# Kernel optimization log

Measured on AMD Instinct MI355X. Metric: run time of the kernel, lower is better.

Reference implementation:

```python
import jax, jax.numpy as jnp
import numpy as np

EPS = 1e-08


def squash(x):
    # x: [..., D]; scale by ||x||^2/(1+||x||^2) and normalize by ||x||
    lengths2 = jnp.sum(x * x, axis=-1, keepdims=True)
    lengths = jnp.sqrt(lengths2)
    return x * (lengths2 / (1.0 + lengths2)) / (lengths + EPS)


def setup_inputs() -> dict:
    key = jax.random.key(0)
    k1, = jax.random.split(key, 1)
    B, G, S, O, D = 32, 8, 1152, 10, 16
    u_predict = jax.random.normal(k1, (B, G, S, O, D), dtype=jnp.float32)
    b_param = jnp.zeros((G, 1, S, O), dtype=jnp.float32)
    return {"u_predict": u_predict, "b_param": b_param, "n_iterations": 3}


def reference(u_predict, b_param, n_iterations):
    B, G, S, O, D = u_predict.shape
    # b: expand param (G,1,S,O) -> (G,B,S,O), permute -> (B,G,S,O)
    b = jnp.transpose(jnp.broadcast_to(b_param, (G, B, S, O)), (1, 0, 2, 3))
    v = None
    for r in range(n_iterations):
        c = jax.nn.softmax(b, axis=3)[..., None]          # [B,G,S,O,1]
        s = jnp.sum(c * u_predict, axis=2)                # [B,G,O,D]
        v = squash(s)                                     # [B,G,O,D]
        if r < n_iterations - 1:
            # agreement: dot(u_predict, v) over D
            b = b + jnp.sum(u_predict * v[:, :, None], axis=-1)  # [B,G,S,O]
    return jnp.sum(v, axis=1)                             # [B,O,D]
```

## Files before the change

kernel.cpp:

```cpp
#include <hip/hip_runtime.h>

#define NB 32
#define NG 8
#define NS 1152
#define NO 10
#define ND 16
#define EPSV 1e-8f

#define THREADS 512
#define NWAVES (THREADS / 64)
#define GRPS (THREADS / 4)
#define NSTEPS (NS / GRPS)

__global__ __launch_bounds__(THREADS)
void AgreementRouting_72988674228343_kernel(const float* __restrict__ u,
                                            const float* __restrict__ b_param,
                                            const int* __restrict__ n_iter_p,
                                            float* __restrict__ out) {
    __shared__ float  b_lds[NS * NO];
    __shared__ float4 sred[NWAVES][NO][4];
    __shared__ float4 v_lds[NO][4];

    const int tid  = threadIdx.x;
    const int blk  = blockIdx.x;
    const int g    = blk & (NG - 1);
    const int bb   = blk >> 3;
    const int wave = tid >> 6;
    const int lane = tid & 63;
    const int d4   = tid & 3;
    const int grp  = tid >> 2;

    const int n_iter = n_iter_p[0];

    const float* bp = b_param + (size_t)g * (NS * NO);
    for (int i = tid; i < NS * NO; i += THREADS) b_lds[i] = bp[i];

    const float4* ub = (const float4*)u + (size_t)blk * (NS * NO * ND / 4);

    float4 v[NO];
    __syncthreads();

    for (int r = 0; r < n_iter; ++r) {
        float4 sacc[NO];
#pragma unroll
        for (int o = 0; o < NO; ++o) sacc[o] = make_float4(0.f, 0.f, 0.f, 0.f);

        for (int step = 0; step < NSTEPS; ++step) {
            const int s = step * GRPS + grp;
            const float4* row = ub + (size_t)s * (NO * 4) + d4;
            float4 uu[NO];
#pragma unroll
            for (int o = 0; o < NO; ++o) uu[o] = row[o * 4];

            float bnew[NO];
            if (r > 0) {
                float p[NO];
#pragma unroll
                for (int o = 0; o < NO; ++o)
                    p[o] = uu[o].x * v[o].x + uu[o].y * v[o].y +
                           uu[o].z * v[o].z + uu[o].w * v[o].w;
#pragma unroll
                for (int o = 0; o < NO; ++o) {
                    p[o] += __shfl_xor(p[o], 1);
                    p[o] += __shfl_xor(p[o], 2);
                    bnew[o] = b_lds[s * NO + o] + p[o];
                }
#pragma unroll
                for (int o = 0; o < NO; ++o)
                    if ((o & 3) == d4) b_lds[s * NO + o] = bnew[o];
            } else {
#pragma unroll
                for (int o = 0; o < NO; ++o) bnew[o] = b_lds[s * NO + o];
            }

            float m = bnew[0];
#pragma unroll
            for (int o = 1; o < NO; ++o) m = fmaxf(m, bnew[o]);
            float e[NO]; float ssum = 0.f;
#pragma unroll
            for (int o = 0; o < NO; ++o) { e[o] = __expf(bnew[o] - m); ssum += e[o]; }
            const float inv = 1.f / ssum;
#pragma unroll
            for (int o = 0; o < NO; ++o) {
                const float c = e[o] * inv;
                sacc[o].x += c * uu[o].x;
                sacc[o].y += c * uu[o].y;
                sacc[o].z += c * uu[o].z;
                sacc[o].w += c * uu[o].w;
            }
        }

#pragma unroll
        for (int o = 0; o < NO; ++o) {
#pragma unroll
            for (int mask = 4; mask <= 32; mask <<= 1) {
                sacc[o].x += __shfl_xor(sacc[o].x, mask);
                sacc[o].y += __shfl_xor(sacc[o].y, mask);
                sacc[o].z += __shfl_xor(sacc[o].z, mask);
                sacc[o].w += __shfl_xor(sacc[o].w, mask);
            }
        }
        if (lane < 4) {
#pragma unroll
            for (int o = 0; o < NO; ++o) sred[wave][o][lane] = sacc[o];
        }
        __syncthreads();

        if (tid < NO * 4) {
            const int o = tid >> 2, dd = tid & 3;
            float4 sv = sred[0][o][dd];
#pragma unroll
            for (int w = 1; w < NWAVES; ++w) {
                float4 t = sred[w][o][dd];
                sv.x += t.x; sv.y += t.y; sv.z += t.z; sv.w += t.w;
            }
            float q = sv.x * sv.x + sv.y * sv.y + sv.z * sv.z + sv.w * sv.w;
            q += __shfl_xor(q, 1);
            q += __shfl_xor(q, 2);
            const float len = sqrtf(q);
            const float f = (q / (1.f + q)) / (len + EPSV);
            const float4 vv = make_float4(sv.x * f, sv.y * f, sv.z * f, sv.w * f);
            v_lds[o][dd] = vv;
            if (r == n_iter - 1) {
                float* op = out + (size_t)bb * (NO * ND) + o * ND + dd * 4;
                atomicAdd(op + 0, vv.x);
                atomicAdd(op + 1, vv.y);
                atomicAdd(op + 2, vv.z);
                atomicAdd(op + 3, vv.w);
            }
        }
        __syncthreads();
#pragma unroll
        for (int o = 0; o < NO; ++o) v[o] = v_lds[o][d4];
    }
}

extern "C" void kernel_launch(void* const* d_in, const int* in_sizes, int n_in,
                              void* d_out, int out_size, void* d_ws, size_t ws_size,
                              hipStream_t stream) {
    const float* u   = (const float*)d_in[0];
    const float* bp  = (const float*)d_in[1];
    const int*   nit = (const int*)d_in[2];
    float* out = (float*)d_out;

    hipMemsetAsync(out, 0, (size_t)out_size * sizeof(float), stream);

    AgreementRouting_72988674228343_kernel<<<dim3(NB * NG), dim3(THREADS), 0, stream>>>(
        u, bp, nit, out);
}
```

Baseline: 318.7 us.

## Stage an fp16 copy of u_predict for later routing iterations

```diff
diff --git a/kernel.cpp b/kernel.cpp
--- a/kernel.cpp
+++ b/kernel.cpp
@@ -1,4 +1,6 @@
 #include <hip/hip_runtime.h>
+#include <hip/hip_fp16.h>
+#include <stdint.h>
 
 #define NB 32
 #define NG 8
@@ -8,81 +10,107 @@
 #define EPSV 1e-8f
 
 #define THREADS 512
-#define NWAVES (THREADS / 64)
 #define GRPS (THREADS / 4)
 #define NSTEPS (NS / GRPS)
+#define UHROW (NO * 4)
+
+typedef float f4v __attribute__((ext_vector_type(4)));
 
 __global__ __launch_bounds__(THREADS)
 void AgreementRouting_72988674228343_kernel(const float* __restrict__ u,
-                                            const float* __restrict__ b_param,
+                                            const float* __restrict__ bparam,
                                             const int* __restrict__ n_iter_p,
-                                            float* __restrict__ out) {
+                                            float* __restrict__ out,
+                                            uint2* __restrict__ uh)
+{
     __shared__ float  b_lds[NS * NO];
-    __shared__ float4 sred[NWAVES][NO][4];
+    __shared__ float4 sred[8][NO][4];
     __shared__ float4 v_lds[NO][4];
 
     const int tid  = threadIdx.x;
-    const int blk  = blockIdx.x;
-    const int g    = blk & (NG - 1);
-    const int bb   = blk >> 3;
+    const int bg   = blockIdx.x;
+    const int g    = bg & 7;
+    const int bb   = bg >> 3;
     const int wave = tid >> 6;
     const int lane = tid & 63;
     const int d4   = tid & 3;
     const int grp  = tid >> 2;
 
-    const int n_iter = n_iter_p[0];
+    const int n = n_iter_p[0];
 
-    const float* bp = b_param + (size_t)g * (NS * NO);
+    const float* bp = bparam + (size_t)g * (NS * NO);
     for (int i = tid; i < NS * NO; i += THREADS) b_lds[i] = bp[i];
+    if (tid < NO * 4) v_lds[tid >> 2][tid & 3] = make_float4(0.f, 0.f, 0.f, 0.f);
 
-    const float4* ub = (const float4*)u + (size_t)blk * (NS * NO * ND / 4);
+    const f4v* ub  = (const f4v*)u + (size_t)bg * (NS * NO * 4);
+    uint2*     uhb = uh + (size_t)bg * (NS * UHROW);
 
-    float4 v[NO];
     __syncthreads();
 
-    for (int r = 0; r < n_iter; ++r) {
+    for (int r = 0; r < n; ++r) {
         float4 sacc[NO];
 #pragma unroll
         for (int o = 0; o < NO; ++o) sacc[o] = make_float4(0.f, 0.f, 0.f, 0.f);
 
         for (int step = 0; step < NSTEPS; ++step) {
             const int s = step * GRPS + grp;
-            const float4* row = ub + (size_t)s * (NO * 4) + d4;
             float4 uu[NO];
+            float bnew[NO];
+
+            if (r == 0) {
+                const f4v* row = ub + (size_t)s * (NO * 4) + d4;
+                f4v t[NO];
 #pragma unroll
-            for (int o = 0; o < NO; ++o) uu[o] = row[o * 4];
-
-            float bnew[NO];
-            if (r > 0) {
-                float p[NO];
+                for (int o = 0; o < NO; ++o) t[o] = __builtin_nontemporal_load(row + o * 4);
+                if (n > 1) {
+                    uint2* wrow = uhb + (size_t)s * UHROW + d4;
 #pragma unroll
-                for (int o = 0; o < NO; ++o)
-                    p[o] = uu[o].x * v[o].x + uu[o].y * v[o].y +
-                           uu[o].z * v[o].z + uu[o].w * v[o].w;
+                    for (int o = 0; o < NO; ++o) {
+                        const __half2 lo = __floats2half2_rn(t[o].x, t[o].y);
+                        const __half2 hi = __floats2half2_rn(t[o].z, t[o].w);
+                        uint2 pk;
+                        pk.x = __builtin_bit_cast(uint32_t, lo);
+                        pk.y = __builtin_bit_cast(uint32_t, hi);
+                        wrow[o * 4] = pk;
+                    }
+                }
 #pragma unroll
                 for (int o = 0; o < NO; ++o) {
-                    p[o] += __shfl_xor(p[o], 1);
-                    p[o] += __shfl_xor(p[o], 2);
-                    bnew[o] = b_lds[s * NO + o] + p[o];
+                    uu[o] = make_float4(t[o].x, t[o].y, t[o].z, t[o].w);
+                    bnew[o] = b_lds[s * NO + o];
+                }
+            } else {
+                const uint2* row = uhb + (size_t)s * UHROW + d4;
+                uint2 pk[NO];
+#pragma unroll
+                for (int o = 0; o < NO; ++o) pk[o] = row[o * 4];
+#pragma unroll
+                for (int o = 0; o < NO; ++o) {
+                    const float2 a = __half22float2(__builtin_bit_cast(__half2, pk[o].x));
+                    const float2 b = __half22float2(__builtin_bit_cast(__half2, pk[o].y));
+                    uu[o] = make_float4(a.x, a.y, b.x, b.y);
                 }
 #pragma unroll
-                for (int o = 0; o < NO; ++o)
-                    if ((o & 3) == d4) b_lds[s * NO + o] = bnew[o];
-            } else {
-#pragma unroll
-                for (int o = 0; o < NO; ++o) bnew[o] = b_lds[s * NO + o];
+                for (int o = 0; o < NO; ++o) {
+                    const float4 vc = v_lds[o][d4];
+                    float p = uu[o].x * vc.x + uu[o].y * vc.y +
+                              uu[o].z * vc.z + uu[o].w * vc.w;
+                    p += __shfl_xor(p, 1);
+                    p += __shfl_xor(p, 2);
+                    bnew[o] = b_lds[s * NO + o] + p;
+                }
             }
 
-            float m = bnew[0];
+            float mx = bnew[0];
 #pragma unroll
-            for (int o = 1; o < NO; ++o) m = fmaxf(m, bnew[o]);
-            float e[NO]; float ssum = 0.f;
+            for (int o = 1; o < NO; ++o) mx = fmaxf(mx, bnew[o]);
+            float ss = 0.f;
 #pragma unroll
-            for (int o = 0; o < NO; ++o) { e[o] = __expf(bnew[o] - m); ssum += e[o]; }
-            const float inv = 1.f / ssum;
+            for (int o = 0; o < NO; ++o) { bnew[o] = __expf(bnew[o] - mx); ss += bnew[o]; }
+            const float inv = 1.f / ss;
 #pragma unroll
             for (int o = 0; o < NO; ++o) {
-                const float c = e[o] * inv;
+                const float c = bnew[o] * inv;
                 sacc[o].x += c * uu[o].x;
                 sacc[o].y += c * uu[o].y;
                 sacc[o].z += c * uu[o].z;
@@ -110,8 +138,8 @@
             const int o = tid >> 2, dd = tid & 3;
             float4 sv = sred[0][o][dd];
 #pragma unroll
-            for (int w = 1; w < NWAVES; ++w) {
-                float4 t = sred[w][o][dd];
+            for (int w = 1; w < 8; ++w) {
+                const float4 t = sred[w][o][dd];
                 sv.x += t.x; sv.y += t.y; sv.z += t.z; sv.w += t.w;
             }
             float q = sv.x * sv.x + sv.y * sv.y + sv.z * sv.z + sv.w * sv.w;
@@ -120,8 +148,10 @@
             const float len = sqrtf(q);
             const float f = (q / (1.f + q)) / (len + EPSV);
             const float4 vv = make_float4(sv.x * f, sv.y * f, sv.z * f, sv.w * f);
-            v_lds[o][dd] = vv;
-            if (r == n_iter - 1) {
+            const float4 c4 = v_lds[o][dd];
+            v_lds[o][dd] = make_float4(c4.x + vv.x, c4.y + vv.y,
+                                       c4.z + vv.z, c4.w + vv.w);
+            if (r == n - 1) {
                 float* op = out + (size_t)bb * (NO * ND) + o * ND + dd * 4;
                 atomicAdd(op + 0, vv.x);
                 atomicAdd(op + 1, vv.y);
@@ -130,8 +160,6 @@
             }
         }
         __syncthreads();
-#pragma unroll
-        for (int o = 0; o < NO; ++o) v[o] = v_lds[o][d4];
     }
 }
 
@@ -142,9 +170,10 @@
     const float* bp  = (const float*)d_in[1];
     const int*   nit = (const int*)d_in[2];
     float* out = (float*)d_out;
+    uint2* uh  = (uint2*)d_ws;
 
     hipMemsetAsync(out, 0, (size_t)out_size * sizeof(float), stream);
 
     AgreementRouting_72988674228343_kernel<<<dim3(NB * NG), dim3(THREADS), 0, stream>>>(
-        u, bp, nit, out);
+        u, bp, nit, out, uh);
 }
```

Measured after the change: 313.2 us. Within noise of the previous version (-1.7%).
